# Performance work log

Measured on AMD Instinct MI355X. Metric: run time of the kernel, lower is better.

The kernel has to match this reference:

```python
import jax, jax.numpy as jnp
import numpy as np

# Dimensions (match init_kwargs / input_specs)
B, C, H, W = 16, 16, 64, 64
N = H * W          # num_nodes
D_E = 64           # node_embed_dim
D_H = 128          # gnn_hidden_dim
D_R = 256          # readout_output_dim


def _param(key, shape, fan_in):
    return jax.random.normal(key, shape, jnp.float32) * (1.0 / np.sqrt(fan_in))


def setup_inputs() -> dict:
    key = jax.random.key(0)
    ks = jax.random.split(key, 16)
    inp = {
        "obs": jax.random.normal(ks[0], (B, C, H, W), jnp.float32),
        # node_embedding MLP (2 layers: C -> D_E -> D_E)
        "e1_w": _param(ks[1], (C, D_E), C),   "e1_b": jnp.zeros((D_E,), jnp.float32),
        "e2_w": _param(ks[2], (D_E, D_E), D_E), "e2_b": jnp.zeros((D_E,), jnp.float32),
        # 3 GNN layers (Linear then adjacency aggregation)
        "g1_w": _param(ks[3], (D_E, D_H), D_E), "g1_b": jnp.zeros((D_H,), jnp.float32),
        "g2_w": _param(ks[4], (D_H, D_H), D_H), "g2_b": jnp.zeros((D_H,), jnp.float32),
        "g3_w": _param(ks[5], (D_H, D_H), D_H), "g3_b": jnp.zeros((D_H,), jnp.float32),
        # readout MLP (2 layers: D_H -> 2*D_H -> D_R)
        "r1_w": _param(ks[6], (D_H, 2 * D_H), D_H),   "r1_b": jnp.zeros((2 * D_H,), jnp.float32),
        "r2_w": _param(ks[7], (2 * D_H, D_R), 2 * D_H), "r2_b": jnp.zeros((D_R,), jnp.float32),
    }
    return inp


def _adj_norm():
    # 4-neighbor grid adjacency on an H x W grid, row-normalized (same for every
    # batch element, so build once as (N, N) instead of (B, N, N)).
    idx = jnp.arange(N)
    up = jnp.eye(N, k=-W, dtype=jnp.float32)                      # i > 0
    down = jnp.eye(N, k=W, dtype=jnp.float32)                     # i < H-1
    left = jnp.eye(N, k=-1, dtype=jnp.float32) * ((idx % W) != 0)[:, None]
    right = jnp.eye(N, k=1, dtype=jnp.float32) * ((idx % W) != (W - 1))[:, None]
    adj = up + down + left + right
    return adj / (adj.sum(axis=1, keepdims=True) + 1e-6)


def reference(obs, e1_w, e1_b, e2_w, e2_b,
              g1_w, g1_b, g2_w, g2_b, g3_w, g3_b,
              r1_w, r1_b, r2_w, r2_b):
    relu = jax.nn.relu
    # grid -> graph: (B, C, H, W) -> (B, N, C)
    x = jnp.transpose(obs, (0, 2, 3, 1)).reshape(B, N, C)
    # node embedding MLP (output activation per ding MLP default)
    h = relu(x @ e1_w + e1_b)
    h = relu(h @ e2_w + e2_b)
    A = _adj_norm()  # (N, N)
    for Wg, bg in ((g1_w, g1_b), (g2_w, g2_b), (g3_w, g3_b)):
        support = h @ Wg + bg                      # (B, N, D_H)
        h = relu(jnp.einsum('nm,bmf->bnf', A, support))
    g = h.mean(axis=1)                              # (B, D_H) graph readout
    g = relu(g @ r1_w + r1_b)
    return relu(g @ r2_w + r2_b)                    # (B, D_R)
```

## Files before the change

### kernel.cpp

```cpp
#include <hip/hip_runtime.h>


typedef __attribute__((ext_vector_type(8))) short bf16x8;
typedef __attribute__((ext_vector_type(4))) float f32x4;
#define MFMA(a, b, c) __builtin_amdgcn_mfma_f32_16x16x32_bf16(a, b, c, 0, 0, 0)

__device__ inline void block_sync_lgkm() {
    asm volatile("" ::: "memory");
    __builtin_amdgcn_s_waitcnt(0xC07F);
    __builtin_amdgcn_s_barrier();
    asm volatile("" ::: "memory");
}

__device__ inline ushort bf16h(float x) {
    unsigned u = __float_as_uint(x);
    return (ushort)((u + 0x7fffu + ((u >> 16) & 1u)) >> 16);
}
__device__ inline void split_bf16(float x, ushort& hi, ushort& lo) {
    hi = bf16h(x);
    lo = bf16h(x - __uint_as_float(((unsigned)hi) << 16));
}
__device__ inline unsigned pack_split(float x) {
    unsigned u = __float_as_uint(x);
    unsigned hi = (u + 0x7fffu + ((u >> 16) & 1u)) >> 16;
    float r = x - __uint_as_float(hi << 16);
    return (hi << 16) | (__float_as_uint(r) >> 16);
}
__device__ inline void frag_packed(const unsigned* bp, bf16x8& bh, bf16x8& bl) {
    unsigned p[8];
#pragma unroll
    for (int j = 0; j < 8; j++) p[j] = bp[j * 65];
    union { bf16x8 v; unsigned d[4]; } H, L;
#pragma unroll
    for (int j = 0; j < 4; j++) {
        const unsigned e = p[2 * j], o = p[2 * j + 1];
        H.d[j] = (o & 0xFFFF0000u) | (e >> 16);
        L.d[j] = (o << 16) | (e & 0xFFFFu);
    }
    bh = H.v; bl = L.v;
}

__global__ __launch_bounds__(256, 4) void prep_embed_kernel(
    const float* __restrict__ obs,
    const float* __restrict__ e1w, const float* __restrict__ e1b,
    const float* __restrict__ e2w, const float* __restrict__ e2b,
    const float* __restrict__ g1w, const float* __restrict__ g2w,
    const float* __restrict__ g3w, ushort* __restrict__ wf,
    float* __restrict__ gsum, float* __restrict__ h0)
{
    const int blk = blockIdx.x, tid = threadIdx.x;

    if (blk < 20) {
        const int u = blk * 4 + (tid >> 6);
        const int l = tid & 63;
        const float* src; int K, kc, t; ushort* dst;
        if (u < 16)      { src = g1w; K = 64;  kc = u >> 3;        t = u & 7; dst = wf + 12288; }
        else if (u < 48) { src = g2w; K = 128; kc = (u - 16) >> 3; t = (u - 16) & 7; dst = wf + 28672; }
        else             { src = g3w; K = 128; kc = (u - 48) >> 3; t = (u - 48) & 7; dst = wf + 61440; }
        ushort* uh = dst + ((kc * 8 + t) * 2 + 0) * 512 + l * 8;
        ushort* ul = dst + ((kc * 8 + t) * 2 + 1) * 512 + l * 8;
        const int f = t * 16 + (l & 15);
        const int kb = kc * 32 + ((l >> 4) << 3);
#pragma unroll
        for (int j = 0; j < 8; j++) {
            const int k = kb + j;
            const float w = (k < K) ? src[k * 128 + f] : 0.f;
            ushort hi, lo; split_bf16(w, hi, lo);
            uh[j] = hi; ul[j] = lo;
        }
        return;
    }
    if (blk < 28) {
        gsum[(blk - 20) * 256 + tid] = 0.f;
        return;
    }

    __shared__ unsigned lds[6240];
    const int eb = blk - 28;
    const int ebid = ((eb & 7) << 7) | (eb >> 3);
    const int b = ebid >> 6, row = ebid & 63;
    const int lane = tid & 63, w = tid >> 6, quad = lane >> 4, nl = lane & 15;
    const int cp = tid >> 4, nq = tid & 15;

    const float4 x4 = *(const float4*)(obs + ((size_t)(b * 16 + cp) << 12) + row * 64 + nq * 4);

    {
        float* wr = (float*)lds;
#pragma unroll
        for (int i = 0; i < 20; i++) {
            const int idx = tid + 256 * i;
            wr[idx] = (idx < 1024) ? e1w[idx] : e2w[idx - 1024];
        }
    }
    __syncthreads();

    bf16x8 e1h, e1l, e2h[2], e2l[2];
    {
        const float* wr = (const float*)lds;
        const int f = 16 * w + nl;
#pragma unroll
        for (int j = 0; j < 8; j++) {
            const int k = quad * 8 + j;
            const float v = (k < 16) ? wr[k * 64 + f] : 0.f;
            ushort hi, lo; split_bf16(v, hi, lo);
            e1h[j] = (short)hi; e1l[j] = (short)lo;
        }
#pragma unroll
        for (int kc = 0; kc < 2; kc++)
#pragma unroll
            for (int j = 0; j < 8; j++) {
                const int k = kc * 32 + quad * 8 + j;
                const float v = wr[1024 + k * 64 + f];
                ushort hi, lo; split_bf16(v, hi, lo);
                e2h[kc][j] = (short)hi; e2l[kc][j] = (short)lo;
            }
    }
    __syncthreads();

    unsigned* Xs = lds;
    unsigned* Hs = lds + 2080;
    {
        unsigned* xp = Xs + cp * 65 + nq * 4;
        xp[0] = pack_split(x4.x); xp[1] = pack_split(x4.y);
        xp[2] = pack_split(x4.z); xp[3] = pack_split(x4.w);
        unsigned* zp = Xs + (16 + cp) * 65 + nq * 4;
        zp[0] = 0u; zp[1] = 0u; zp[2] = 0u; zp[3] = 0u;
    }
    __syncthreads();

#pragma unroll
    for (int nt = 0; nt < 4; nt++) {
        const unsigned* bp = Xs + (quad * 8) * 65 + nt * 16 + nl;
        bf16x8 bh, bl; frag_packed(bp, bh, bl);
        f32x4 c = {0.f, 0.f, 0.f, 0.f};
        c = MFMA(e1h, bh, c); c = MFMA(e1h, bl, c); c = MFMA(e1l, bh, c);
#pragma unroll
        for (int reg = 0; reg < 4; reg++) {
            const int fm = 16 * w + quad * 4 + reg;
            Hs[fm * 65 + nt * 16 + nl] = pack_split(fmaxf(c[reg] + e1b[fm], 0.f));
        }
    }
    __syncthreads();

    f32x4 a2[4];
#pragma unroll
    for (int nt = 0; nt < 4; nt++) a2[nt] = (f32x4){0.f, 0.f, 0.f, 0.f};
#pragma unroll
    for (int kc = 0; kc < 2; kc++) {
#pragma unroll
        for (int nt = 0; nt < 4; nt++) {
            const unsigned* bp = Hs + (kc * 32 + quad * 8) * 65 + nt * 16 + nl;
            bf16x8 bh, bl; frag_packed(bp, bh, bl);
            a2[nt] = MFMA(e2h[kc], bh, a2[nt]);
            a2[nt] = MFMA(e2h[kc], bl, a2[nt]);
            a2[nt] = MFMA(e2l[kc], bh, a2[nt]);
        }
    }
#pragma unroll
    for (int reg = 0; reg < 4; reg++) {
        const int f = 16 * w + quad * 4 + reg;
        const float bv = e2b[f];
#pragma unroll
        for (int nt = 0; nt < 4; nt++)
            h0[((size_t)(b * 64 + f) << 12) + row * 64 + nt * 16 + nl] =
                fmaxf(a2[nt][reg] + bv, 0.f);
    }
}

template <int K, bool MEAN>
__global__ __launch_bounds__(256, 4) void gnn_kernel(
    const float* __restrict__ hin, const ushort* __restrict__ wf,
    const float* __restrict__ bias, float* __restrict__ hout,
    float* __restrict__ gsum)
{
    constexpr int NQ = K / 32;
    __shared__ unsigned As[2][32 * 65];
    const int tid = threadIdx.x;
    const int bid = ((blockIdx.x & 7) << 7) | (blockIdx.x >> 3);
    const int b = bid >> 6, row = bid & 63;
    const int lane = tid & 63, w = tid >> 6, quad = lane >> 4, nl = lane & 15;
    const int kp = tid >> 4, nq = tid & 15;
    const float* hb = hin + (size_t)b * K * 4096;
    const int rowu = (row > 0) ? row - 1 : row;
    const int rowd = (row < 63) ? row + 1 : row;
    const float su = (row > 0) ? 1.f : 0.f;
    const float sd = (row < 63) ? 1.f : 0.f;
    float inv[4];
#pragma unroll
    for (int i = 0; i < 4; i++) {
        const int n = nq * 4 + i;
        const int deg = (row > 0) + (row < 63) + (n > 0) + (n < 63);
        inv[i] = 1.f / ((float)deg + 1e-6f);
    }

    const ushort* wfl = wf + lane * 8;
    f32x4 acc[4][2];
#pragma unroll
    for (int nt = 0; nt < 4; nt++) {
        acc[nt][0] = (f32x4){0.f, 0.f, 0.f, 0.f};
        acc[nt][1] = (f32x4){0.f, 0.f, 0.f, 0.f};
    }

    float4 S[6];
    bf16x8 V[2][2];

    auto sload = [&](int q) {
#pragma unroll
        for (int it = 0; it < 2; it++) {
            const int kg = q * 32 + it * 16 + kp;
            const float* pk = hb + ((size_t)kg << 12) + nq * 4;
            S[it * 3 + 0] = *(const float4*)(pk + row * 64);
            S[it * 3 + 1] = *(const float4*)(pk + rowu * 64);
            S[it * 3 + 2] = *(const float4*)(pk + rowd * 64);
        }
    };
    auto wload = [&](int q) {
#pragma unroll
        for (int ftl = 0; ftl < 2; ftl++) {
            V[ftl][0] = *(const bf16x8*)(wfl + ((q * 8 + 2 * w + ftl) * 2) * 512);
            V[ftl][1] = *(const bf16x8*)(wfl + ((q * 8 + 2 * w + ftl) * 2 + 1) * 512);
        }
    };
    auto stage = [&](unsigned* Ab) {
#pragma unroll
        for (int it = 0; it < 2; it++) {
            const int kl = it * 16 + kp;
            const float4 c4 = S[it * 3 + 0];
            const float4 u4 = S[it * 3 + 1];
            const float4 d4 = S[it * 3 + 2];
            const float pw = __shfl_up(c4.w, 1);
            const float nx = __shfl_down(c4.x, 1);
            const float lx = (nq > 0) ? pw : 0.f;
            const float rw = (nq < 15) ? nx : 0.f;
            unsigned* ap = Ab + kl * 65 + nq * 4;
            ap[0] = pack_split((su * u4.x + sd * d4.x + lx + c4.y) * inv[0]);
            ap[1] = pack_split((su * u4.y + sd * d4.y + c4.x + c4.z) * inv[1]);
            ap[2] = pack_split((su * u4.z + sd * d4.z + c4.y + c4.w) * inv[2]);
            ap[3] = pack_split((su * u4.w + sd * d4.w + c4.z + rw) * inv[3]);
        }
    };
    auto consume = [&](const unsigned* Ab) {
#pragma unroll
        for (int nt = 0; nt < 4; nt++) {
            const unsigned* bp = Ab + (quad * 8) * 65 + nt * 16 + nl;
            bf16x8 bh, bl; frag_packed(bp, bh, bl);
            acc[nt][0] = MFMA(V[0][0], bh, acc[nt][0]);
            acc[nt][0] = MFMA(V[0][0], bl, acc[nt][0]);
            acc[nt][0] = MFMA(V[0][1], bh, acc[nt][0]);
            acc[nt][1] = MFMA(V[1][0], bh, acc[nt][1]);
            acc[nt][1] = MFMA(V[1][0], bl, acc[nt][1]);
            acc[nt][1] = MFMA(V[1][1], bh, acc[nt][1]);
        }
    };

    wload(0);
    sload(0);
    stage(As[0]);
    sload(1);
    block_sync_lgkm();

#pragma unroll
    for (int q = 0; q < NQ; q++) {
        consume(As[q & 1]);
        if (q + 1 < NQ) {
            wload(q + 1);
            stage(As[(q + 1) & 1]);
            if (q + 2 < NQ) sload(q + 2);
            block_sync_lgkm();
        }
    }

    if (!MEAN) {
#pragma unroll
        for (int ftl = 0; ftl < 2; ftl++) {
            const int fb = 32 * w + 16 * ftl + quad * 4;
            const float b0 = bias[fb], b1 = bias[fb + 1], b2 = bias[fb + 2], b3 = bias[fb + 3];
#pragma unroll
            for (int nt = 0; nt < 4; nt++) {
                const int n = 16 * nt + nl;
                const int deg = (row > 0) + (row < 63) + (n > 0) + (n < 63);
                const float rs = (float)deg / ((float)deg + 1e-6f);
                float* op = hout + ((size_t)(b * 128 + fb) << 12) + row * 64 + n;
                op[0]        = fmaxf(acc[nt][ftl][0] + rs * b0, 0.f);
                op[1u << 12] = fmaxf(acc[nt][ftl][1] + rs * b1, 0.f);
                op[2u << 12] = fmaxf(acc[nt][ftl][2] + rs * b2, 0.f);
                op[3u << 12] = fmaxf(acc[nt][ftl][3] + rs * b3, 0.f);
            }
        }
    } else {
#pragma unroll
        for (int ftl = 0; ftl < 2; ftl++) {
            const int fb = 32 * w + 16 * ftl + quad * 4;
#pragma unroll
            for (int reg = 0; reg < 4; reg++) {
                const float bv = bias[fb + reg];
                float v = 0.f;
#pragma unroll
                for (int nt = 0; nt < 4; nt++) {
                    const int n = 16 * nt + nl;
                    const int deg = (row > 0) + (row < 63) + (n > 0) + (n < 63);
                    const float rs = (float)deg / ((float)deg + 1e-6f);
                    v += fmaxf(acc[nt][ftl][reg] + rs * bv, 0.f);
                }
                v += __shfl_xor(v, 1); v += __shfl_xor(v, 2);
                v += __shfl_xor(v, 4); v += __shfl_xor(v, 8);
                if (nl == 0) atomicAdd(&gsum[b * 128 + fb + reg], v * (1.f / 4096.f));
            }
        }
    }
}

__global__ __launch_bounds__(256) void readout_kernel(
    const float* __restrict__ gsum, const float* __restrict__ r1w,
    const float* __restrict__ r1b, const float* __restrict__ r2w,
    const float* __restrict__ r2b, float* __restrict__ out)
{
    __shared__ float gs[128];
    __shared__ float g2[256];
    const int b = blockIdx.x, tid = threadIdx.x;
    if (tid < 128) gs[tid] = gsum[b * 128 + tid];
    __syncthreads();
    float a = r1b[tid];
#pragma unroll 16
    for (int k = 0; k < 128; k++) a = fmaf(gs[k], r1w[k * 256 + tid], a);
    g2[tid] = fmaxf(a, 0.f);
    __syncthreads();
    float a2 = r2b[tid];
#pragma unroll 16
    for (int k = 0; k < 256; k++) a2 = fmaf(g2[k], r2w[k * 256 + tid], a2);
    out[b * 256 + tid] = fmaxf(a2, 0.f);
}

extern "C" void kernel_launch(void* const* d_in, const int* in_sizes, int n_in,
                              void* d_out, int out_size, void* d_ws, size_t ws_size,
                              hipStream_t stream)
{
    const float* obs = (const float*)d_in[0];
    const float* e1w = (const float*)d_in[1];
    const float* e1b = (const float*)d_in[2];
    const float* e2w = (const float*)d_in[3];
    const float* e2b = (const float*)d_in[4];
    const float* g1w = (const float*)d_in[5];
    const float* g1b = (const float*)d_in[6];
    const float* g2w = (const float*)d_in[7];
    const float* g2b = (const float*)d_in[8];
    const float* g3w = (const float*)d_in[9];
    const float* g3b = (const float*)d_in[10];
    const float* r1w = (const float*)d_in[11];
    const float* r1b = (const float*)d_in[12];
    const float* r2w = (const float*)d_in[13];
    const float* r2b = (const float*)d_in[14];
    float* out = (float*)d_out;
    float* ws = (float*)d_ws;

    float* h0 = ws;
    float* h1 = ws + 4194304;
    float* h2 = ws + 4194304 + 8388608;
    float* gsum = (float*)((char*)d_ws + 80u * 1024u * 1024u);
    ushort* wfb = (ushort*)((char*)d_ws + 80u * 1024u * 1024u + 8192u);

    hipLaunchKernelGGL(prep_embed_kernel, dim3(1052), dim3(256), 0, stream,
                       obs, e1w, e1b, e2w, e2b, g1w, g2w, g3w, wfb, gsum, h0);
    hipLaunchKernelGGL((gnn_kernel<64, false>), dim3(1024), dim3(256), 0, stream,
                       h0, wfb + 12288, g1b, h1, nullptr);
    hipLaunchKernelGGL((gnn_kernel<128, false>), dim3(1024), dim3(256), 0, stream,
                       h1, wfb + 28672, g2b, h2, nullptr);
    hipLaunchKernelGGL((gnn_kernel<128, true>), dim3(1024), dim3(256), 0, stream,
                       h2, wfb + 61440, g3b, nullptr, gsum);
    hipLaunchKernelGGL(readout_kernel, dim3(16), dim3(256), 0, stream,
                       gsum, r1w, r1b, r2w, r2b, out);
}
```

Measured before the change: 158.2 us.

## Stage full K aggregation tile in LDS then run MFMA loop with single barrier

Replaces the double-buffered per-32-K staging pipeline, which had a barrier every chunk, with a two-phase scheme. First the whole aggregated K-by-64 tile is computed and written to LDS using a two-deep register prefetch of global loads. Then a single __syncthreads precedes a barrier-free MFMA loop with double-buffered weight fragments. This removes the per-chunk barriers but raises LDS use to K*65 words (about 33KB for K=128), which may limit occupancy at 4 blocks per CU, and it loses the overlap between staging and MFMA.

```diff
diff --git a/kernel.cpp b/kernel.cpp
--- a/kernel.cpp
+++ b/kernel.cpp
@@ -4,13 +4,6 @@
 typedef __attribute__((ext_vector_type(8))) short bf16x8;
 typedef __attribute__((ext_vector_type(4))) float f32x4;
 #define MFMA(a, b, c) __builtin_amdgcn_mfma_f32_16x16x32_bf16(a, b, c, 0, 0, 0)
-
-__device__ inline void block_sync_lgkm() {
-    asm volatile("" ::: "memory");
-    __builtin_amdgcn_s_waitcnt(0xC07F);
-    __builtin_amdgcn_s_barrier();
-    asm volatile("" ::: "memory");
-}
 
 __device__ inline ushort bf16h(float x) {
     unsigned u = __float_as_uint(x);
@@ -173,8 +166,9 @@
     const float* __restrict__ bias, float* __restrict__ hout,
     float* __restrict__ gsum)
 {
-    constexpr int NQ = K / 32;
-    __shared__ unsigned As[2][32 * 65];
+    constexpr int KC = K / 32;
+    constexpr int NIT = K / 16;
+    __shared__ unsigned As[K * 65];
     const int tid = threadIdx.x;
     const int bid = ((blockIdx.x & 7) << 7) | (blockIdx.x >> 3);
     const int b = bid >> 6, row = bid & 63;
@@ -201,73 +195,63 @@
         acc[nt][1] = (f32x4){0.f, 0.f, 0.f, 0.f};
     }
 
-    float4 S[6];
-    bf16x8 V[2][2];
-
-    auto sload = [&](int q) {
-#pragma unroll
-        for (int it = 0; it < 2; it++) {
-            const int kg = q * 32 + it * 16 + kp;
+    {
+        float4 c4[2], u4[2], d4[2];
+        auto ld = [&](int g, int s) {
+            const int kg = g * 16 + kp;
             const float* pk = hb + ((size_t)kg << 12) + nq * 4;
-            S[it * 3 + 0] = *(const float4*)(pk + row * 64);
-            S[it * 3 + 1] = *(const float4*)(pk + rowu * 64);
-            S[it * 3 + 2] = *(const float4*)(pk + rowd * 64);
-        }
-    };
-    auto wload = [&](int q) {
-#pragma unroll
-        for (int ftl = 0; ftl < 2; ftl++) {
-            V[ftl][0] = *(const bf16x8*)(wfl + ((q * 8 + 2 * w + ftl) * 2) * 512);
-            V[ftl][1] = *(const bf16x8*)(wfl + ((q * 8 + 2 * w + ftl) * 2 + 1) * 512);
-        }
-    };
-    auto stage = [&](unsigned* Ab) {
-#pragma unroll
-        for (int it = 0; it < 2; it++) {
-            const int kl = it * 16 + kp;
-            const float4 c4 = S[it * 3 + 0];
-            const float4 u4 = S[it * 3 + 1];
-            const float4 d4 = S[it * 3 + 2];
-            const float pw = __shfl_up(c4.w, 1);
-            const float nx = __shfl_down(c4.x, 1);
+            c4[s] = *(const float4*)(pk + row * 64);
+            u4[s] = *(const float4*)(pk + rowu * 64);
+            d4[s] = *(const float4*)(pk + rowd * 64);
+        };
+        auto st = [&](int g, int s) {
+            const int kg = g * 16 + kp;
+            const float pw = __shfl_up(c4[s].w, 1);
+            const float nx = __shfl_down(c4[s].x, 1);
             const float lx = (nq > 0) ? pw : 0.f;
             const float rw = (nq < 15) ? nx : 0.f;
-            unsigned* ap = Ab + kl * 65 + nq * 4;
-            ap[0] = pack_split((su * u4.x + sd * d4.x + lx + c4.y) * inv[0]);
-            ap[1] = pack_split((su * u4.y + sd * d4.y + c4.x + c4.z) * inv[1]);
-            ap[2] = pack_split((su * u4.z + sd * d4.z + c4.y + c4.w) * inv[2]);
-            ap[3] = pack_split((su * u4.w + sd * d4.w + c4.z + rw) * inv[3]);
+            unsigned* ap = As + kg * 65 + nq * 4;
+            ap[0] = pack_split((su * u4[s].x + sd * d4[s].x + lx + c4[s].y) * inv[0]);
+            ap[1] = pack_split((su * u4[s].y + sd * d4[s].y + c4[s].x + c4[s].z) * inv[1]);
+            ap[2] = pack_split((su * u4[s].z + sd * d4[s].z + c4[s].y + c4[s].w) * inv[2]);
+            ap[3] = pack_split((su * u4[s].w + sd * d4[s].w + c4[s].z + rw) * inv[3]);
+        };
+        ld(0, 0);
+        ld(1, 1);
+#pragma unroll
+        for (int g = 0; g < NIT; g++) {
+            st(g, g & 1);
+            if (g + 2 < NIT) ld(g + 2, g & 1);
+        }
+    }
+
+    bf16x8 V[2][2][2];
+    auto wload = [&](int kc) {
+#pragma unroll
+        for (int ftl = 0; ftl < 2; ftl++) {
+            V[kc & 1][ftl][0] = *(const bf16x8*)(wfl + ((kc * 8 + 2 * w + ftl) * 2) * 512);
+            V[kc & 1][ftl][1] = *(const bf16x8*)(wfl + ((kc * 8 + 2 * w + ftl) * 2 + 1) * 512);
         }
     };
-    auto consume = [&](const unsigned* Ab) {
+    wload(0);
+    if (KC > 1) wload(1);
+    __syncthreads();
+
+#pragma unroll
+    for (int kc = 0; kc < KC; kc++) {
+        const bf16x8 (*Vr)[2] = V[kc & 1];
 #pragma unroll
         for (int nt = 0; nt < 4; nt++) {
-            const unsigned* bp = Ab + (quad * 8) * 65 + nt * 16 + nl;
+            const unsigned* bp = As + (kc * 32 + quad * 8) * 65 + nt * 16 + nl;
             bf16x8 bh, bl; frag_packed(bp, bh, bl);
-            acc[nt][0] = MFMA(V[0][0], bh, acc[nt][0]);
-            acc[nt][0] = MFMA(V[0][0], bl, acc[nt][0]);
-            acc[nt][0] = MFMA(V[0][1], bh, acc[nt][0]);
-            acc[nt][1] = MFMA(V[1][0], bh, acc[nt][1]);
-            acc[nt][1] = MFMA(V[1][0], bl, acc[nt][1]);
-            acc[nt][1] = MFMA(V[1][1], bh, acc[nt][1]);
-        }
-    };
-
-    wload(0);
-    sload(0);
-    stage(As[0]);
-    sload(1);
-    block_sync_lgkm();
-
-#pragma unroll
-    for (int q = 0; q < NQ; q++) {
-        consume(As[q & 1]);
-        if (q + 1 < NQ) {
-            wload(q + 1);
-            stage(As[(q + 1) & 1]);
-            if (q + 2 < NQ) sload(q + 2);
-            block_sync_lgkm();
-        }
+            acc[nt][0] = MFMA(Vr[0][0], bh, acc[nt][0]);
+            acc[nt][0] = MFMA(Vr[0][0], bl, acc[nt][0]);
+            acc[nt][0] = MFMA(Vr[0][1], bh, acc[nt][0]);
+            acc[nt][1] = MFMA(Vr[1][0], bh, acc[nt][1]);
+            acc[nt][1] = MFMA(Vr[1][0], bl, acc[nt][1]);
+            acc[nt][1] = MFMA(Vr[1][1], bh, acc[nt][1]);
+        }
+        if (kc + 2 < KC) wload(kc + 2);
     }
 
     if (!MEAN) {
```

New measurement: 161.4 us. Within noise of the previous version (+2.0%).

## Fuse readout MLP into last GNN layer via last-block atomic counter

Applied to the files above, without the earlier changes.

Drops the separate readout kernel launch. The final GNN kernel now increments a global counter after its gsum atomics, and the last 16 blocks to arrive spin until all 1024 blocks have finished. Each of those blocks then computes the two-layer readout MLP for one batch element. This removes one launch and its gap between kernels, at the cost of a grid-wide spin wait that assumes those waiting blocks cannot starve blocks that have not yet been scheduled.

```diff
diff --git a/kernel.cpp b/kernel.cpp
--- a/kernel.cpp
+++ b/kernel.cpp
@@ -46,7 +46,8 @@
     const float* __restrict__ e2w, const float* __restrict__ e2b,
     const float* __restrict__ g1w, const float* __restrict__ g2w,
     const float* __restrict__ g3w, ushort* __restrict__ wf,
-    float* __restrict__ gsum, float* __restrict__ h0)
+    float* __restrict__ gsum, unsigned* __restrict__ cnt,
+    float* __restrict__ h0)
 {
     const int blk = blockIdx.x, tid = threadIdx.x;
 
@@ -72,6 +73,8 @@
     }
     if (blk < 28) {
         gsum[(blk - 20) * 256 + tid] = 0.f;
+        if (blk == 27 && tid == 0)
+            __hip_atomic_store(cnt, 0u, __ATOMIC_RELAXED, __HIP_MEMORY_SCOPE_AGENT);
         return;
     }
 
@@ -171,7 +174,10 @@
 __global__ __launch_bounds__(256, 4) void gnn_kernel(
     const float* __restrict__ hin, const ushort* __restrict__ wf,
     const float* __restrict__ bias, float* __restrict__ hout,
-    float* __restrict__ gsum)
+    float* __restrict__ gsum, unsigned* __restrict__ cnt,
+    const float* __restrict__ r1w, const float* __restrict__ r1b,
+    const float* __restrict__ r2w, const float* __restrict__ r2b,
+    float* __restrict__ out)
 {
     constexpr int NQ = K / 32;
     __shared__ unsigned As[2][32 * 65];
@@ -307,28 +313,39 @@
                 if (nl == 0) atomicAdd(&gsum[b * 128 + fb + reg], v * (1.f / 4096.f));
             }
         }
-    }
-}
-
-__global__ __launch_bounds__(256) void readout_kernel(
-    const float* __restrict__ gsum, const float* __restrict__ r1w,
-    const float* __restrict__ r1b, const float* __restrict__ r2w,
-    const float* __restrict__ r2b, float* __restrict__ out)
-{
-    __shared__ float gs[128];
-    __shared__ float g2[256];
-    const int b = blockIdx.x, tid = threadIdx.x;
-    if (tid < 128) gs[tid] = gsum[b * 128 + tid];
-    __syncthreads();
-    float a = r1b[tid];
+
+        __shared__ unsigned rank_s;
+        __threadfence();
+        __syncthreads();
+        if (tid == 0)
+            rank_s = __hip_atomic_fetch_add(cnt, 1u, __ATOMIC_ACQ_REL, __HIP_MEMORY_SCOPE_AGENT);
+        __syncthreads();
+        const unsigned rank = rank_s;
+        if (rank >= 1008u) {
+            if (tid == 0) {
+                while (__hip_atomic_load(cnt, __ATOMIC_ACQUIRE, __HIP_MEMORY_SCOPE_AGENT) < 1024u)
+                    __builtin_amdgcn_s_sleep(8);
+            }
+            __syncthreads();
+            __threadfence();
+            const int rb = (int)(rank - 1008u);
+            float* gs = (float*)As;
+            float* g2 = gs + 128;
+            if (tid < 128)
+                gs[tid] = __hip_atomic_load(&gsum[rb * 128 + tid],
+                                            __ATOMIC_RELAXED, __HIP_MEMORY_SCOPE_AGENT);
+            __syncthreads();
+            float a = r1b[tid];
 #pragma unroll 16
-    for (int k = 0; k < 128; k++) a = fmaf(gs[k], r1w[k * 256 + tid], a);
-    g2[tid] = fmaxf(a, 0.f);
-    __syncthreads();
-    float a2 = r2b[tid];
+            for (int k = 0; k < 128; k++) a = fmaf(gs[k], r1w[k * 256 + tid], a);
+            g2[tid] = fmaxf(a, 0.f);
+            __syncthreads();
+            float a2 = r2b[tid];
 #pragma unroll 16
-    for (int k = 0; k < 256; k++) a2 = fmaf(g2[k], r2w[k * 256 + tid], a2);
-    out[b * 256 + tid] = fmaxf(a2, 0.f);
+            for (int k = 0; k < 256; k++) a2 = fmaf(g2[k], r2w[k * 256 + tid], a2);
+            out[rb * 256 + tid] = fmaxf(a2, 0.f);
+        }
+    }
 }
 
 extern "C" void kernel_launch(void* const* d_in, const int* in_sizes, int n_in,
@@ -358,15 +375,17 @@
     float* h2 = ws + 4194304 + 8388608;
     float* gsum = (float*)((char*)d_ws + 80u * 1024u * 1024u);
     ushort* wfb = (ushort*)((char*)d_ws + 80u * 1024u * 1024u + 8192u);
+    unsigned* cnt = (unsigned*)((char*)d_ws + 80u * 1024u * 1024u + 200u * 1024u);
 
     hipLaunchKernelGGL(prep_embed_kernel, dim3(1052), dim3(256), 0, stream,
-                       obs, e1w, e1b, e2w, e2b, g1w, g2w, g3w, wfb, gsum, h0);
+                       obs, e1w, e1b, e2w, e2b, g1w, g2w, g3w, wfb, gsum, cnt, h0);
     hipLaunchKernelGGL((gnn_kernel<64, false>), dim3(1024), dim3(256), 0, stream,
-                       h0, wfb + 12288, g1b, h1, nullptr);
+                       h0, wfb + 12288, g1b, h1, nullptr, nullptr,
+                       nullptr, nullptr, nullptr, nullptr, nullptr);
     hipLaunchKernelGGL((gnn_kernel<128, false>), dim3(1024), dim3(256), 0, stream,
-                       h1, wfb + 28672, g2b, h2, nullptr);
+                       h1, wfb + 28672, g2b, h2, nullptr, nullptr,
+                       nullptr, nullptr, nullptr, nullptr, nullptr);
     hipLaunchKernelGGL((gnn_kernel<128, true>), dim3(1024), dim3(256), 0, stream,
-                       h2, wfb + 61440, g3b, nullptr, gsum);
-    hipLaunchKernelGGL(readout_kernel, dim3(16), dim3(256), 0, stream,
-                       gsum, r1w, r1b, r2w, r2b, out);
-}
+                       h2, wfb + 61440, g3b, nullptr, gsum, cnt,
+                       r1w, r1b, r2w, r2b, out);
+}
```

New measurement: 237.5 us. 50.1% more time.
